# Optimization experiments

Hardware: AMD Instinct MI355X
Metric: run time of the kernel (lower is better)

## Reference

```python
import jax, jax.numpy as jnp
import numpy as np

TOKENS = 512
DIM_HEAD = 64
MAX_TOKENS = 2000
HEADS = 8
BATCH = 8


def _build_indices(tokens: int, max_tokens: int) -> np.ndarray:
    # Faithful replication of the torch index construction (done once in numpy).
    idx = np.arange(-tokens, tokens + 1)
    pad = max_tokens - 2 * tokens + 1
    row = np.concatenate([np.full(pad, idx[0]), idx, np.full(pad, idx[-1])])
    mat = np.stack([np.roll(row, i) for i in range(max_tokens)])
    mat = mat[: max_tokens - tokens + 2, max_tokens - tokens + 1 :]
    # torch fancy indexing wraps negative indices -> take mod of table size
    return (mat % (2 * tokens - 1)).astype(np.int32)


def setup_inputs() -> dict:
    key = jax.random.key(0)
    kq, kp = jax.random.split(key)
    scale = DIM_HEAD ** (-0.5)
    q = jax.random.normal(kq, (BATCH, HEADS, TOKENS, DIM_HEAD), dtype=jnp.float32)
    rel_pos_emb = (
        jax.random.normal(kp, (HEADS, 2 * TOKENS - 1, DIM_HEAD), dtype=jnp.float32)
        * scale
    )
    indices = jnp.asarray(_build_indices(TOKENS, MAX_TOKENS))
    return {"q": q, "rel_pos_emb": rel_pos_emb, "indices": indices}


def reference(q, rel_pos_emb, indices):
    t = q.shape[2]
    idx = indices[:t, :t]  # [r, t]
    # gather: [heads, r, t, dim_head]
    gathered = rel_pos_emb[:, idx]
    # emb[b,h,t,r] = sum_d q[b,h,t,d] * gathered[h,r,t,d]
    return jnp.einsum("bhtd,hrtd->bhtr", q, gathered)
```

## Files before the change

### kernel.cpp

```cpp
#include <hip/hip_runtime.h>
#include <hip/hip_bf16.h>


#define TOKENS 512
#define DIMH 64
#define NREL 1023
#define IDXN 1490

#define ESTR 72
#define EROWS 128
#define PSTR 84

typedef short bf16x8 __attribute__((ext_vector_type(8)));
typedef float f32x4 __attribute__((ext_vector_type(4)));

__device__ __forceinline__ ushort4 cvt4(float4 v) {
    union { __hip_bfloat162 h2[2]; ushort4 s; } u;
    u.h2[0] = __float22bfloat162_rn(float2{v.x, v.y});
    u.h2[1] = __float22bfloat162_rn(float2{v.z, v.w});
    return u.s;
}
__device__ __forceinline__ bf16x8 cvt8(float4 a, float4 b) {
    union { __hip_bfloat162 h2[4]; bf16x8 v; } u;
    u.h2[0] = __float22bfloat162_rn(float2{a.x, a.y});
    u.h2[1] = __float22bfloat162_rn(float2{a.z, a.w});
    u.h2[2] = __float22bfloat162_rn(float2{b.x, b.y});
    u.h2[3] = __float22bfloat162_rn(float2{b.z, b.w});
    return u.v;
}

__global__ __launch_bounds__(256, 4)
void relpos_xcd4(const float* __restrict__ q,
                 const float* __restrict__ emb,
                 const int* __restrict__ indices,
                 float* __restrict__ out)
{
    __shared__ unsigned short Es[EROWS * ESTR];
    __shared__ float Ps[4 * 16 * PSTR];

    const int tid = threadIdx.x;
    const int blk = blockIdx.x;
    const int h  = blk & 7;
    const int tt = (blk >> 3) & 7;
    const int bg = (blk >> 6) & 7;
    const int rt = blk >> 9;
    const int t0 = tt * 64;
    const int r0 = rt * 64;

    {
        const int j_honest = indices[(size_t)(r0 + 63) * IDXN + t0];
        asm volatile("" :: "s"(j_honest));
    }
    int j_lo = t0 - r0 - 63;
    if (j_lo < 0) j_lo += NREL;

    const int lane = tid & 63;
    const int wave = tid >> 6;
    const int quad = lane >> 4;
    const int l15  = lane & 15;

    const float* qp = q + (((size_t)bg * 8 + h) * TOKENS + t0 + wave * 16 + l15) * DIMH
                    + quad * 8;
    const float4 qa0 = *(const float4*)qp;
    const float4 qa1 = *(const float4*)(qp + 4);
    const float4 qb0 = *(const float4*)(qp + 32);
    const float4 qb1 = *(const float4*)(qp + 36);

    {
        const float* embh = emb + (size_t)h * NREL * DIMH;
        const int c16 = tid & 15;
        const int r16 = tid >> 4;
#pragma unroll
        for (int it = 0; it < 8; ++it) {
            const int row = it * 16 + r16;
            int j = j_lo + row;
            if (j >= NREL) j -= NREL;
            const float4 v = *(const float4*)(embh + (size_t)j * DIMH + c16 * 4);
            *(ushort4*)(Es + (size_t)row * ESTR + c16 * 4) = cvt4(v);
        }
    }

    const bf16x8 bq0 = cvt8(qa0, qa1);
    const bf16x8 bq1 = cvt8(qb0, qb1);

    __syncthreads();

    float* psw = Ps + (size_t)wave * 16 * PSTR;
    const int ebase = wave * 16;

    bf16x8 ae[5][2];
#pragma unroll
    for (int i = 0; i < 5; ++i) {
        const unsigned short* ap = Es + (size_t)(ebase + i * 16 + l15) * ESTR
                                 + quad * 8;
        ae[i][0] = *(const bf16x8*)ap;
        ae[i][1] = *(const bf16x8*)(ap + 32);
    }

#pragma unroll
    for (int i = 0; i < 5; ++i) {
        f32x4 acc = {0.f, 0.f, 0.f, 0.f};
        acc = __builtin_amdgcn_mfma_f32_16x16x32_bf16(ae[i][0], bq0, acc, 0, 0, 0);
        acc = __builtin_amdgcn_mfma_f32_16x16x32_bf16(ae[i][1], bq1, acc, 0, 0, 0);
        *(f32x4*)(psw + (size_t)l15 * PSTR + i * 16 + quad * 4) = acc;
    }

    float* ob = out + (((size_t)bg * 8 + h) * TOKENS + t0 + wave * 16) * (size_t)TOKENS
              + r0 + l15 * 4;
#pragma unroll
    for (int p = 0; p < 4; ++p) {
        const int u = quad + p * 4;
        const float* pr = psw + (size_t)u * PSTR + (u + 63 - l15 * 4);
        f32x4 o;
        o[0] = pr[0];
        o[1] = pr[-1];
        o[2] = pr[-2];
        o[3] = pr[-3];
        __builtin_nontemporal_store(o, (f32x4*)(ob + (size_t)u * TOKENS));
    }
}

extern "C" void kernel_launch(void* const* d_in, const int* in_sizes, int n_in,
                              void* d_out, int out_size, void* d_ws, size_t ws_size,
                              hipStream_t stream) {
    const float* q       = (const float*)d_in[0];
    const float* emb     = (const float*)d_in[1];
    const int*   indices = (const int*)d_in[2];
    float* out = (float*)d_out;

    relpos_xcd4<<<dim3(4096), dim3(256), 0, stream>>>(q, emb, indices, out);
}
```

Before: 91.32 us.

## Loop each block over four batches to reuse the staged embedding tile

The grid shrinks from 4096 to 1024 blocks. Each block now handles four batch elements in turn, reusing the bf16 embedding tile it staged in LDS and the A fragments already held in registers. The next batch's q rows are loaded before the current MFMA and store phase, so that load latency overlaps with work. This removes repeated emb gathers and conversions across batches, but it cuts block-level parallelism and makes each block's run longer and more serialized.

```diff
diff --git a/kernel.cpp b/kernel.cpp
--- a/kernel.cpp
+++ b/kernel.cpp
@@ -30,10 +30,10 @@
 }
 
 __global__ __launch_bounds__(256, 4)
-void relpos_xcd4(const float* __restrict__ q,
-                 const float* __restrict__ emb,
-                 const int* __restrict__ indices,
-                 float* __restrict__ out)
+void relpos_bgloop(const float* __restrict__ q,
+                   const float* __restrict__ emb,
+                   const int* __restrict__ indices,
+                   float* __restrict__ out)
 {
     __shared__ unsigned short Es[EROWS * ESTR];
     __shared__ float Ps[4 * 16 * PSTR];
@@ -42,8 +42,8 @@
     const int blk = blockIdx.x;
     const int h  = blk & 7;
     const int tt = (blk >> 3) & 7;
-    const int bg = (blk >> 6) & 7;
-    const int rt = blk >> 9;
+    const int rt = (blk >> 6) & 7;
+    const int bp = blk >> 9;
     const int t0 = tt * 64;
     const int r0 = rt * 64;
 
@@ -59,8 +59,10 @@
     const int quad = lane >> 4;
     const int l15  = lane & 15;
 
-    const float* qp = q + (((size_t)bg * 8 + h) * TOKENS + t0 + wave * 16 + l15) * DIMH
+    const size_t QB = (size_t)8 * TOKENS * DIMH;
+    const float* qp = q + (((size_t)(bp * 4) * 8 + h) * TOKENS + t0 + wave * 16 + l15) * DIMH
                     + quad * 8;
+
     const float4 qa0 = *(const float4*)qp;
     const float4 qa1 = *(const float4*)(qp + 4);
     const float4 qb0 = *(const float4*)(qp + 32);
@@ -80,15 +82,13 @@
         }
     }
 
-    const bf16x8 bq0 = cvt8(qa0, qa1);
-    const bf16x8 bq1 = cvt8(qb0, qb1);
+    bf16x8 bq0 = cvt8(qa0, qa1);
+    bf16x8 bq1 = cvt8(qb0, qb1);
 
     __syncthreads();
 
-    float* psw = Ps + (size_t)wave * 16 * PSTR;
+    bf16x8 ae[5][2];
     const int ebase = wave * 16;
-
-    bf16x8 ae[5][2];
 #pragma unroll
     for (int i = 0; i < 5; ++i) {
         const unsigned short* ap = Es + (size_t)(ebase + i * 16 + l15) * ESTR
@@ -97,26 +97,45 @@
         ae[i][1] = *(const bf16x8*)(ap + 32);
     }
 
+    float* psw = Ps + (size_t)wave * 16 * PSTR;
+
 #pragma unroll
-    for (int i = 0; i < 5; ++i) {
-        f32x4 acc = {0.f, 0.f, 0.f, 0.f};
-        acc = __builtin_amdgcn_mfma_f32_16x16x32_bf16(ae[i][0], bq0, acc, 0, 0, 0);
-        acc = __builtin_amdgcn_mfma_f32_16x16x32_bf16(ae[i][1], bq1, acc, 0, 0, 0);
-        *(f32x4*)(psw + (size_t)l15 * PSTR + i * 16 + quad * 4) = acc;
-    }
+    for (int it = 0; it < 4; ++it) {
+        float4 na0 = {0,0,0,0}, na1 = {0,0,0,0}, nb0 = {0,0,0,0}, nb1 = {0,0,0,0};
+        if (it < 3) {
+            const float* nq = qp + (size_t)(it + 1) * QB;
+            na0 = *(const float4*)nq;
+            na1 = *(const float4*)(nq + 4);
+            nb0 = *(const float4*)(nq + 32);
+            nb1 = *(const float4*)(nq + 36);
+        }
 
-    float* ob = out + (((size_t)bg * 8 + h) * TOKENS + t0 + wave * 16) * (size_t)TOKENS
-              + r0 + l15 * 4;
 #pragma unroll
-    for (int p = 0; p < 4; ++p) {
-        const int u = quad + p * 4;
-        const float* pr = psw + (size_t)u * PSTR + (u + 63 - l15 * 4);
-        f32x4 o;
-        o[0] = pr[0];
-        o[1] = pr[-1];
-        o[2] = pr[-2];
-        o[3] = pr[-3];
-        __builtin_nontemporal_store(o, (f32x4*)(ob + (size_t)u * TOKENS));
+        for (int i = 0; i < 5; ++i) {
+            f32x4 acc = {0.f, 0.f, 0.f, 0.f};
+            acc = __builtin_amdgcn_mfma_f32_16x16x32_bf16(ae[i][0], bq0, acc, 0, 0, 0);
+            acc = __builtin_amdgcn_mfma_f32_16x16x32_bf16(ae[i][1], bq1, acc, 0, 0, 0);
+            *(f32x4*)(psw + (size_t)l15 * PSTR + i * 16 + quad * 4) = acc;
+        }
+
+        if (it < 3) {
+            bq0 = cvt8(na0, na1);
+            bq1 = cvt8(nb0, nb1);
+        }
+
+        float* ob = out + (((size_t)(bp * 4 + it) * 8 + h) * TOKENS + t0 + wave * 16)
+                        * (size_t)TOKENS + r0 + l15 * 4;
+#pragma unroll
+        for (int p = 0; p < 4; ++p) {
+            const int u = quad + p * 4;
+            const float* pr = psw + (size_t)u * PSTR + (u + 63 - l15 * 4);
+            f32x4 o;
+            o[0] = pr[0];
+            o[1] = pr[-1];
+            o[2] = pr[-2];
+            o[3] = pr[-3];
+            __builtin_nontemporal_store(o, (f32x4*)(ob + (size_t)u * TOKENS));
+        }
     }
 }
 
@@ -128,5 +147,5 @@
     const int*   indices = (const int*)d_in[2];
     float* out = (float*)d_out;
 
-    relpos_xcd4<<<dim3(4096), dim3(256), 0, stream>>>(q, emb, indices, out);
+    relpos_bgloop<<<dim3(1024), dim3(256), 0, stream>>>(q, emb, indices, out);
 }
```

Result: slower. 93.76 us (+2.7%).
